# Kernel tuning notes

Measured on AMD Instinct MI355X. Metric: run time of the kernel, lower is better.

The kernel has to match this reference:

```python
import jax, jax.numpy as jnp
import numpy as np

B, L, H, P = 4, 4096, 1024, 256


def _bin_op(ei, ej):
    A_i, Bu_i = ei
    A_j, Bu_j = ej
    return (A_j * A_i, A_j * Bu_i + Bu_j)


def _s5(x, log_real, imag, B_real, B_imag, C_real, C_imag, D, log_Delta):
    Lam = jax.lax.complex(-jnp.exp(log_real), imag)                 # [P]
    B_tilde = jax.lax.complex(B_real, B_imag)                        # [P,H]
    C_tilde = jax.lax.complex(C_real, C_imag)                        # [H,P]
    Delta = jnp.exp(log_Delta)                                       # [P]
    Lambda_bar = jnp.exp(Lam * Delta)                                # [P]
    Lam_safe = jnp.where(jnp.abs(Lam) < 1e-6,
                         jnp.full_like(Lam, 1e-6), Lam)
    B_bar = ((Lambda_bar - 1.0) / Lam_safe)[:, None] * B_tilde       # [P,H]
    Bu = x.astype(jnp.complex64) @ B_bar.T                           # [B,L,P]
    La = jnp.broadcast_to(Lambda_bar[None, None, :], Bu.shape)
    _, xs = jax.lax.associative_scan(_bin_op, (La, Bu), axis=1)      # [B,L,P]
    ys = jnp.real(xs @ C_tilde.T) + D * x                            # [B,L,H]
    return jax.nn.gelu(ys, approximate=False)


def setup_inputs() -> dict:
    key = jax.random.key(0)
    ks = jax.random.split(key, 17)
    std_b = 1.0 / H ** 0.5
    std_c = 1.0 / P ** 0.5
    d = {"x": jax.random.normal(ks[0], (B, L, H), dtype=jnp.float32)}
    for i, pfx in enumerate(["fwd", "bwd"]):
        o = 1 + 8 * i
        d[pfx + "_log_real"] = jax.random.normal(ks[o], (P,)) * 0.5
        d[pfx + "_imag"] = jax.random.normal(ks[o + 1], (P,))
        d[pfx + "_B_real"] = jax.random.normal(ks[o + 2], (P, H)) * std_b
        d[pfx + "_B_imag"] = jax.random.normal(ks[o + 3], (P, H)) * std_b
        d[pfx + "_C_real"] = jax.random.normal(ks[o + 4], (H, P)) * std_c
        d[pfx + "_C_imag"] = jax.random.normal(ks[o + 5], (H, P)) * std_c
        d[pfx + "_D"] = jnp.ones((H,), dtype=jnp.float32)
        d[pfx + "_log_Delta"] = jnp.zeros((P,), dtype=jnp.float32)
    return d


def reference(x,
              fwd_log_real, fwd_imag, fwd_B_real, fwd_B_imag,
              fwd_C_real, fwd_C_imag, fwd_D, fwd_log_Delta,
              bwd_log_real, bwd_imag, bwd_B_real, bwd_B_imag,
              bwd_C_real, bwd_C_imag, bwd_D, bwd_log_Delta):
    y_f = _s5(x, fwd_log_real, fwd_imag, fwd_B_real, fwd_B_imag,
              fwd_C_real, fwd_C_imag, fwd_D, fwd_log_Delta)
    x_flip = jnp.flip(x, axis=1)
    y_b = _s5(x_flip, bwd_log_real, bwd_imag, bwd_B_real, bwd_B_imag,
              bwd_C_real, bwd_C_imag, bwd_D, bwd_log_Delta)
    return y_f + jnp.flip(y_b, axis=1)
```

## Files before the change

### kernel.cpp

```cpp
#include <hip/hip_runtime.h>
#include <math.h>


typedef short bf16x8 __attribute__((ext_vector_type(8)));
typedef float f32x4 __attribute__((ext_vector_type(4)));
typedef unsigned short u16x8 __attribute__((ext_vector_type(8)));

__device__ __forceinline__ unsigned short f2bf(float f) {
  union { float f; unsigned int u; } v; v.f = f;
  unsigned int r = (v.u + 0x7FFFu + ((v.u >> 16) & 1u)) >> 16;
  return (unsigned short)r;
}
__device__ __forceinline__ float bf2f(unsigned short s) {
  union { unsigned int u; float f; } v; v.u = ((unsigned int)s) << 16;
  return v.f;
}
__device__ __forceinline__ float gelu_fast(float v) {
  const float u = 1.5957691216057308f * fmaf(0.044715f * v, v * v, v);
  return v / (1.f + __expf(-u));
}
__device__ __forceinline__ void gload16(const unsigned short* g, void* l) {
  __builtin_amdgcn_global_load_lds(
      (const __attribute__((address_space(1))) void*)g,
      (__attribute__((address_space(3))) void*)l, 16, 0, 0);
}

__global__ __launch_bounds__(256) void cast_prep_kernel(
    const float* __restrict__ x, unsigned short* __restrict__ xbf,
    const float* __restrict__ flr, const float* __restrict__ fim,
    const float* __restrict__ fBr, const float* __restrict__ fBi,
    const float* __restrict__ fCr, const float* __restrict__ fCi,
    const float* __restrict__ flD,
    const float* __restrict__ blr, const float* __restrict__ bim,
    const float* __restrict__ bBr, const float* __restrict__ bBi,
    const float* __restrict__ bCr, const float* __restrict__ bCi,
    const float* __restrict__ blD,
    unsigned short* __restrict__ W, unsigned short* __restrict__ CmT,
    float4* __restrict__ lamp) {
  const int tid = threadIdx.x;
  if (blockIdx.x < 8192) {
    const size_t i = (size_t)blockIdx.x * 256 + tid;
    const float4* xv = (const float4*)x;
    float4 a = xv[2 * i], b = xv[2 * i + 1];
    u16x8 r;
    r[0] = f2bf(a.x); r[1] = f2bf(a.y); r[2] = f2bf(a.z); r[3] = f2bf(a.w);
    r[4] = f2bf(b.x); r[5] = f2bf(b.y); r[6] = f2bf(b.z); r[7] = f2bf(b.w);
    *(u16x8*)(xbf + 8 * i) = r;
    return;
  }
  const int bid = blockIdx.x - 8192;
  if (bid < 512) {
    const int dir = bid >> 8, p = bid & 255;
    const float* lr_ = dir ? blr : flr;
    const float* im_ = dir ? bim : fim;
    const float* lD_ = dir ? blD : flD;
    const float* Br_ = dir ? bBr : fBr;
    const float* Bi_ = dir ? bBi : fBi;
    const float Lre = -expf(lr_[p]);
    const float Lim = im_[p];
    const float Dl = expf(lD_[p]);
    const float ar = Lre * Dl, ai = Lim * Dl;
    const float er = expf(ar);
    const float lre = er * cosf(ai), lim = er * sinf(ai);
    const float e64 = expf(64.f * ar);
    const float l64re = e64 * cosf(64.f * ai), l64im = e64 * sinf(64.f * ai);
    float sre = Lre, sim = Lim;
    if (sqrtf(Lre * Lre + Lim * Lim) < 1e-6f) { sre = 1e-6f; sim = 0.f; }
    const float den = sre * sre + sim * sim;
    const float fre = ((lre - 1.f) * sre + lim * sim) / den;
    const float fi2 = (lim * sre - (lre - 1.f) * sim) / den;
    if (tid == 0) lamp[dir * 256 + p] = make_float4(lre, lim, l64re, l64im);
    const size_t rowR = (size_t)(dir * 512 + 2 * p) * 1024;
    const size_t rowI = rowR + 1024;
    for (int h = tid; h < 1024; h += 256) {
      const float Br = Br_[p * 1024 + h], Bi = Bi_[p * 1024 + h];
      W[rowR + h] = f2bf(fre * Br - fi2 * Bi);
      W[rowI + h] = f2bf(fre * Bi + fi2 * Br);
    }
  } else {
    const int h = bid - 512;
    for (int k = tid; k < 1024; k += 256) {
      const int dir = k >> 9, within = k & 511;
      const int p = within >> 1, comp = within & 1;
      const float* C = comp ? (dir ? bCi : fCi) : (dir ? bCr : fCr);
      float v = C[(size_t)h * 256 + p];
      if (comp) v = -v;
      CmT[(size_t)h * 1024 + k] = f2bf(v);
    }
  }
}

#define GEMM_KSTEP(ACC, KT, APTR, BPTR)                                        \
  {                                                                            \
    const int k0 = (KT) << 6;                                                  \
    _Pragma("unroll") for (int i = 0; i < 4; ++i) {                            \
      const int r = (i << 5) + tr;                                             \
      const int o = (i << 12) + (tid << 4);                                    \
      gload16(APTR + (size_t)(m0 + r) * 1024 + (k0 + csw), (char*)As + o);     \
      gload16(BPTR + (size_t)(n0 + r) * 1024 + (k0 + csw), (char*)Bs + o);     \
    }                                                                          \
    __syncthreads();                                                           \
    _Pragma("unroll") for (int kk = 0; kk < 64; kk += 32) {                    \
      bf16x8 af[4], bf_[4];                                                    \
      _Pragma("unroll") for (int m4 = 0; m4 < 4; ++m4) {                       \
        const int row = (wm << 6) + (m4 << 4) + fr;                            \
        af[m4] = *(const bf16x8*)&As[row * 64 + ((kk + ks) ^ sw)];             \
      }                                                                        \
      _Pragma("unroll") for (int n4 = 0; n4 < 4; ++n4) {                       \
        const int row = (wn << 6) + (n4 << 4) + fr;                            \
        bf_[n4] = *(const bf16x8*)&Bs[row * 64 + ((kk + ks) ^ sw)];            \
      }                                                                        \
      _Pragma("unroll") for (int m4 = 0; m4 < 4; ++m4)                         \
          _Pragma("unroll") for (int n4 = 0; n4 < 4; ++n4)                     \
              ACC[m4][n4] = __builtin_amdgcn_mfma_f32_16x16x32_bf16(           \
                  af[m4], bf_[n4], ACC[m4][n4], 0, 0, 0);                      \
    }                                                                          \
    __syncthreads();                                                           \
  }

__global__ __launch_bounds__(256) void gemm1_kernel(
    const unsigned short* __restrict__ xbf, const unsigned short* __restrict__ W,
    unsigned short* __restrict__ Zb) {
  __shared__ unsigned short As[128 * 64];
  __shared__ unsigned short Bs[128 * 64];
  const int tid = threadIdx.x;
  const int lane = tid & 63;
  const int w = tid >> 6;
  const int wm = w >> 1, wn = w & 1;
  const int fr = lane & 15;
  const int ks = (lane >> 4) << 3;
  const int sw = (fr & 7) << 3;
  const int tr = tid >> 3;
  const int csw = ((tid & 7) ^ (tr & 7)) << 3;
  const int bsw = ((blockIdx.x & 7) << 7) + (blockIdx.x >> 3);
  const int nt = bsw & 7, mt = bsw >> 3;
  const int m0 = mt << 7, n0 = nt << 7;

  f32x4 acc[4][4] = {};

  for (int kt = 0; kt < 16; ++kt) GEMM_KSTEP(acc, kt, xbf, W);

  const int rb = (lane >> 4) << 2;
#pragma unroll
  for (int m4 = 0; m4 < 4; ++m4)
#pragma unroll
    for (int n4 = 0; n4 < 4; ++n4) {
      const size_t gn = n0 + (wn << 6) + (n4 << 4) + fr;
#pragma unroll
      for (int r = 0; r < 4; ++r) {
        const size_t gm = m0 + (wm << 6) + (m4 << 4) + rb + r;
        Zb[gm * 1024 + gn] = f2bf(acc[m4][n4][r]);
      }
    }
}

__global__ __launch_bounds__(256) void scanA_kernel(
    unsigned int* __restrict__ Zp, const float4* __restrict__ lamp,
    float2* __restrict__ part) {
  const int p = threadIdx.x;
  const int k = blockIdx.x & 63;
  const int s = blockIdx.x >> 6;
  const int dir = s & 1, b = s >> 1;
  const float4 lp = lamp[dir * 256 + p];
  const float lre = lp.x, lim = lp.y;
  const size_t col = (size_t)dir * 256 + p;
  const size_t mbase = (size_t)b * 4096 + (size_t)k * 64;
  float sre = 0.f, sim = 0.f;
  if (dir == 0) {
    for (int i = 0; i < 64; ++i) {
      const size_t idx = (mbase + i) * 512 + col;
      const unsigned int u = Zp[idx];
      const float nr = fmaf(lre, sre, fmaf(-lim, sim, bf2f((unsigned short)u)));
      const float ni = fmaf(lre, sim, fmaf(lim, sre, bf2f((unsigned short)(u >> 16))));
      sre = nr; sim = ni;
      Zp[idx] = (unsigned int)f2bf(sre) | ((unsigned int)f2bf(sim) << 16);
    }
  } else {
    for (int i = 63; i >= 0; --i) {
      const size_t idx = (mbase + i) * 512 + col;
      const unsigned int u = Zp[idx];
      const float nr = fmaf(lre, sre, fmaf(-lim, sim, bf2f((unsigned short)u)));
      const float ni = fmaf(lre, sim, fmaf(lim, sre, bf2f((unsigned short)(u >> 16))));
      sre = nr; sim = ni;
      Zp[idx] = (unsigned int)f2bf(sre) | ((unsigned int)f2bf(sim) << 16);
    }
  }
  part[(size_t)(s * 64 + k) * 256 + p] = make_float2(sre, sim);
}

__global__ __launch_bounds__(256) void scanC_kernel(
    const unsigned int* __restrict__ Zp, const float4* __restrict__ lamp,
    const float2* __restrict__ part, unsigned int* __restrict__ xsbf) {
  const int p = threadIdx.x;
  const int k = blockIdx.x & 63;
  const int s = blockIdx.x >> 6;
  const int dir = s & 1, b = s >> 1;
  const float4 lp = lamp[dir * 256 + p];
  const float lre = lp.x, lim = lp.y, wr64 = lp.z, wi64 = lp.w;
  const size_t col = (size_t)dir * 256 + p;
  const size_t mbase = (size_t)b * 4096 + (size_t)k * 64;

  float cr = 0.f, ci = 0.f, wr = 1.f, wi = 0.f;
  if (dir == 0) {
    for (int j = k - 1; j >= 0; --j) {
      const float2 S = part[(size_t)(s * 64 + j) * 256 + p];
      cr = fmaf(wr, S.x, fmaf(-wi, S.y, cr));
      ci = fmaf(wr, S.y, fmaf(wi, S.x, ci));
      const float t = wr * wr64 - wi * wi64;
      wi = wr * wi64 + wi * wr64; wr = t;
    }
  } else {
    for (int j = k + 1; j < 64; ++j) {
      const float2 S = part[(size_t)(s * 64 + j) * 256 + p];
      cr = fmaf(wr, S.x, fmaf(-wi, S.y, cr));
      ci = fmaf(wr, S.y, fmaf(wi, S.x, ci));
      const float t = wr * wr64 - wi * wi64;
      wi = wr * wi64 + wi * wr64; wr = t;
    }
  }

  float qr = lre * cr - lim * ci;
  float qi = lre * ci + lim * cr;
  if (dir == 0) {
    for (int i = 0; i < 64; ++i) {
      const size_t idx = (mbase + i) * 512 + col;
      const unsigned int u = Zp[idx];
      const float vr = bf2f((unsigned short)u) + qr;
      const float vi = bf2f((unsigned short)(u >> 16)) + qi;
      xsbf[idx] = (unsigned int)f2bf(vr) | ((unsigned int)f2bf(vi) << 16);
      const float t = lre * qr - lim * qi;
      qi = lre * qi + lim * qr; qr = t;
    }
  } else {
    for (int i = 63; i >= 0; --i) {
      const size_t idx = (mbase + i) * 512 + col;
      const unsigned int u = Zp[idx];
      const float vr = bf2f((unsigned short)u) + qr;
      const float vi = bf2f((unsigned short)(u >> 16)) + qi;
      xsbf[idx] = (unsigned int)f2bf(vr) | ((unsigned int)f2bf(vi) << 16);
      const float t = lre * qr - lim * qi;
      qi = lre * qi + lim * qr; qr = t;
    }
  }
}

__global__ __launch_bounds__(256, 2) void gemm2_kernel(
    const unsigned short* __restrict__ A2, const unsigned short* __restrict__ CmT,
    const unsigned short* __restrict__ xbf, const float* __restrict__ Df,
    const float* __restrict__ Db, float* __restrict__ out) {
  __shared__ unsigned short As[128 * 64];
  __shared__ unsigned short Bs[128 * 64];
  const int tid = threadIdx.x;
  const int lane = tid & 63;
  const int w = tid >> 6;
  const int wm = w >> 1, wn = w & 1;
  const int fr = lane & 15;
  const int ks = (lane >> 4) << 3;
  const int sw = (fr & 7) << 3;
  const int tr = tid >> 3;
  const int csw = ((tid & 7) ^ (tr & 7)) << 3;
  const int bsw = ((blockIdx.x & 7) << 7) + (blockIdx.x >> 3);
  const int nt = bsw & 7, mt = bsw >> 3;
  const int m0 = mt << 7, n0 = nt << 7;

  f32x4 accf[4][4] = {};
  f32x4 accb[4][4] = {};

  for (int kt = 0; kt < 8; ++kt) GEMM_KSTEP(accf, kt, A2, CmT);
  for (int kt = 8; kt < 16; ++kt) GEMM_KSTEP(accb, kt, A2, CmT);

  const int rb = (lane >> 4) << 2;
#pragma unroll
  for (int n4 = 0; n4 < 4; ++n4) {
    const size_t gn = n0 + (wn << 6) + (n4 << 4) + fr;
    const float dfv = Df[gn], dbv = Db[gn];
#pragma unroll
    for (int m4 = 0; m4 < 4; ++m4) {
#pragma unroll
      for (int r = 0; r < 4; ++r) {
        const size_t gm = m0 + (wm << 6) + (m4 << 4) + rb + r;
        const float xv = bf2f(xbf[gm * 1024 + gn]);
        out[gm * 1024 + gn] = gelu_fast(accf[m4][n4][r] + dfv * xv) +
                              gelu_fast(accb[m4][n4][r] + dbv * xv);
      }
    }
  }
}

extern "C" void kernel_launch(void* const* d_in, const int* in_sizes, int n_in,
                              void* d_out, int out_size, void* d_ws, size_t ws_size,
                              hipStream_t stream) {
  const float* x = (const float*)d_in[0];
  const float* flr = (const float*)d_in[1];
  const float* fim = (const float*)d_in[2];
  const float* fBr = (const float*)d_in[3];
  const float* fBi = (const float*)d_in[4];
  const float* fCr = (const float*)d_in[5];
  const float* fCi = (const float*)d_in[6];
  const float* fD  = (const float*)d_in[7];
  const float* flD = (const float*)d_in[8];
  const float* blr = (const float*)d_in[9];
  const float* bim = (const float*)d_in[10];
  const float* bBr = (const float*)d_in[11];
  const float* bBi = (const float*)d_in[12];
  const float* bCr = (const float*)d_in[13];
  const float* bCi = (const float*)d_in[14];
  const float* bD  = (const float*)d_in[15];
  const float* blD = (const float*)d_in[16];

  char* ws = (char*)d_ws;
  unsigned short* xbf  = (unsigned short*)(ws);
  unsigned short* W    = (unsigned short*)(ws + 33554432);
  unsigned short* CmT  = (unsigned short*)(ws + 35651584);
  unsigned short* Zb   = (unsigned short*)(ws + 37748736);
  unsigned short* xsbf = (unsigned short*)(ws + 71303168);
  float4*         lamp = (float4*)(ws + 104857600);
  float2*         part = (float2*)(ws + 104865792);

  dim3 blk(256);
  cast_prep_kernel<<<9728, blk, 0, stream>>>(
      x, xbf, flr, fim, fBr, fBi, fCr, fCi, flD,
      blr, bim, bBr, bBi, bCr, bCi, blD, W, CmT, lamp);
  gemm1_kernel<<<1024, blk, 0, stream>>>(xbf, W, Zb);
  scanA_kernel<<<512, blk, 0, stream>>>((unsigned int*)Zb, lamp, part);
  scanC_kernel<<<512, blk, 0, stream>>>((unsigned int*)Zb, lamp, part,
                                        (unsigned int*)xsbf);
  gemm2_kernel<<<1024, blk, 0, stream>>>(xsbf, CmT, xbf, fD, bD, (float*)d_out);
}
```

Measured before the change: 155.5 us.

## Double-buffer LDS tiles in both GEMMs to overlap global loads with MFMA

Both GEMM kernels now keep two LDS buffers and issue the next k-tile's global-to-LDS loads before computing on the current tile. A partial vmcnt wait (8 outstanding loads) plus a barrier publishes the current tile, replacing the full sync-load-sync sequence per k-step. This is meant to hide global memory latency behind MFMA work. In exchange it doubles LDS usage to 64KB per block, which may reduce occupancy, especially for gemm2 with its launch bound of 2 blocks per CU.

```diff
diff --git a/kernel.cpp b/kernel.cpp
--- a/kernel.cpp
+++ b/kernel.cpp
@@ -90,39 +90,53 @@
   }
 }
 
-#define GEMM_KSTEP(ACC, KT, APTR, BPTR)                                        \
+#define GEMM_STAGE(BUF, KT, APTR, BPTR)                                        \
   {                                                                            \
     const int k0 = (KT) << 6;                                                  \
     _Pragma("unroll") for (int i = 0; i < 4; ++i) {                            \
       const int r = (i << 5) + tr;                                             \
-      const int o = (i << 12) + (tid << 4);                                    \
+      const int o = ((BUF) << 14) + (i << 12) + (tid << 4);                    \
       gload16(APTR + (size_t)(m0 + r) * 1024 + (k0 + csw), (char*)As + o);     \
       gload16(BPTR + (size_t)(n0 + r) * 1024 + (k0 + csw), (char*)Bs + o);     \
     }                                                                          \
-    __syncthreads();                                                           \
+  }
+
+#define GEMM_COMPUTE(BUF, ACC)                                                 \
+  {                                                                            \
+    const int bo = (BUF) << 13;               \
     _Pragma("unroll") for (int kk = 0; kk < 64; kk += 32) {                    \
       bf16x8 af[4], bf_[4];                                                    \
       _Pragma("unroll") for (int m4 = 0; m4 < 4; ++m4) {                       \
         const int row = (wm << 6) + (m4 << 4) + fr;                            \
-        af[m4] = *(const bf16x8*)&As[row * 64 + ((kk + ks) ^ sw)];             \
+        af[m4] = *(const bf16x8*)&As[bo + row * 64 + ((kk + ks) ^ sw)];        \
       }                                                                        \
       _Pragma("unroll") for (int n4 = 0; n4 < 4; ++n4) {                       \
         const int row = (wn << 6) + (n4 << 4) + fr;                            \
-        bf_[n4] = *(const bf16x8*)&Bs[row * 64 + ((kk + ks) ^ sw)];            \
+        bf_[n4] = *(const bf16x8*)&Bs[bo + row * 64 + ((kk + ks) ^ sw)];       \
       }                                                                        \
       _Pragma("unroll") for (int m4 = 0; m4 < 4; ++m4)                         \
           _Pragma("unroll") for (int n4 = 0; n4 < 4; ++n4)                     \
               ACC[m4][n4] = __builtin_amdgcn_mfma_f32_16x16x32_bf16(           \
                   af[m4], bf_[n4], ACC[m4][n4], 0, 0, 0);                      \
     }                                                                          \
-    __syncthreads();                                                           \
-  }
+  }
+
+#define PIPE_PUBLISH8()                                                        \
+  asm volatile("s_waitcnt vmcnt(8)" ::: "memory");                             \
+  __builtin_amdgcn_sched_barrier(0);                                           \
+  __builtin_amdgcn_s_barrier();                                                \
+  __builtin_amdgcn_sched_barrier(0);
+
+#define PIPE_CLOSE()                                                           \
+  __builtin_amdgcn_sched_barrier(0);                                           \
+  __builtin_amdgcn_s_barrier();                                                \
+  __builtin_amdgcn_sched_barrier(0);
 
 __global__ __launch_bounds__(256) void gemm1_kernel(
     const unsigned short* __restrict__ xbf, const unsigned short* __restrict__ W,
     unsigned short* __restrict__ Zb) {
-  __shared__ unsigned short As[128 * 64];
-  __shared__ unsigned short Bs[128 * 64];
+  __shared__ unsigned short As[2 * 128 * 64];
+  __shared__ unsigned short Bs[2 * 128 * 64];
   const int tid = threadIdx.x;
   const int lane = tid & 63;
   const int w = tid >> 6;
@@ -138,7 +152,17 @@
 
   f32x4 acc[4][4] = {};
 
-  for (int kt = 0; kt < 16; ++kt) GEMM_KSTEP(acc, kt, xbf, W);
+  GEMM_STAGE(0, 0, xbf, W);
+  int cur = 0;
+  for (int kt = 0; kt < 15; ++kt) {
+    GEMM_STAGE(cur ^ 1, kt + 1, xbf, W);
+    PIPE_PUBLISH8();
+    GEMM_COMPUTE(cur, acc);
+    PIPE_CLOSE();
+    cur ^= 1;
+  }
+  __syncthreads();
+  GEMM_COMPUTE(cur, acc);
 
   const int rb = (lane >> 4) << 2;
 #pragma unroll
@@ -248,8 +272,8 @@
     const unsigned short* __restrict__ A2, const unsigned short* __restrict__ CmT,
     const unsigned short* __restrict__ xbf, const float* __restrict__ Df,
     const float* __restrict__ Db, float* __restrict__ out) {
-  __shared__ unsigned short As[128 * 64];
-  __shared__ unsigned short Bs[128 * 64];
+  __shared__ unsigned short As[2 * 128 * 64];
+  __shared__ unsigned short Bs[2 * 128 * 64];
   const int tid = threadIdx.x;
   const int lane = tid & 63;
   const int w = tid >> 6;
@@ -266,8 +290,26 @@
   f32x4 accf[4][4] = {};
   f32x4 accb[4][4] = {};
 
-  for (int kt = 0; kt < 8; ++kt) GEMM_KSTEP(accf, kt, A2, CmT);
-  for (int kt = 8; kt < 16; ++kt) GEMM_KSTEP(accb, kt, A2, CmT);
+  GEMM_STAGE(0, 0, A2, CmT);
+  int cur = 0;
+#pragma unroll
+  for (int kt = 0; kt < 8; ++kt) {
+    GEMM_STAGE(cur ^ 1, kt + 1, A2, CmT);
+    PIPE_PUBLISH8();
+    GEMM_COMPUTE(cur, accf);
+    PIPE_CLOSE();
+    cur ^= 1;
+  }
+#pragma unroll
+  for (int kt = 8; kt < 15; ++kt) {
+    GEMM_STAGE(cur ^ 1, kt + 1, A2, CmT);
+    PIPE_PUBLISH8();
+    GEMM_COMPUTE(cur, accb);
+    PIPE_CLOSE();
+    cur ^= 1;
+  }
+  __syncthreads();
+  GEMM_COMPUTE(cur, accb);
 
   const int rb = (lane >> 4) << 2;
 #pragma unroll
```

Measured after the change: 151.2 us. 1.03x faster.
